# Optimization experiments

Measured on AMD Instinct MI355X. Metric: run time of the kernel, lower is better.

The kernel has to match this reference:

```python
import jax, jax.numpy as jnp
import numpy as np

B, T, N, C = 2, 3, 6, 16            # batch, time steps, cameras, frustum channels
FD, FH, FW = 48, 24, 64             # frustum depth bins, feature height, width
GX, GY, GZ = 100, 100, 8            # voxel grid size (X, Y, Z)
PC_MIN = np.array([-50.0, -50.0, -3.0], np.float32)
PC_MAX = np.array([50.0, 50.0, 5.0], np.float32)
D_MIN, D_MAX = 2.0, 46.8            # uniform depth discretization (UD)
OUT_CH = 40


def setup_inputs() -> dict:
    key = jax.random.key(0)
    ks = jax.random.split(key, 8)
    frustum_features = jax.random.normal(ks[0], (B, T, N, C, FD, FH, FW), jnp.float32)
    # camera looks along world +x so voxel points land in front of the camera
    base_rt = jnp.array([[0., -1., 0., 0.],
                         [0., 0., -1., 0.],
                         [1., 0., 0., 0.],
                         [0., 0., 0., 1.]], jnp.float32)
    RT = base_rt + 0.02 * jax.random.normal(ks[1], (B, T, N, 4, 4), jnp.float32)
    K = jnp.array([[32., 0., FW / 2.], [0., 32., FH / 2.], [0., 0., 1.]], jnp.float32)
    intrins = K + 0.1 * jax.random.normal(ks[2], (B, 3, 3), jnp.float32)
    DoF = jnp.eye(4, dtype=jnp.float32) + 0.01 * jax.random.normal(ks[3], (B, T, 4, 4), jnp.float32)
    W_N = 0.05 * jax.random.normal(ks[4], (OUT_CH, N * C), jnp.float32)
    b_N = jnp.zeros((OUT_CH,), jnp.float32)
    W_T = 0.05 * jax.random.normal(ks[5], (OUT_CH, T * OUT_CH), jnp.float32)
    b_T = jnp.zeros((OUT_CH,), jnp.float32)
    return {"frustum_features": frustum_features, "RT": RT, "intrins": intrins,
            "DoF": DoF, "W_N": W_N, "b_N": b_N, "W_T": W_T, "b_T": b_T}


def _grid_sample_3d(feat, grid):
    """Trilinear grid_sample. feat [M,C,D,H,W], grid [M,A,B2,C3,3] with
    normalized (x->W, y->H, z->D) coords, align_corners=True, zeros padding."""
    def one(f, g):
        _, Dd, Hh, Ww = f.shape
        ix = (g[..., 0] + 1.) * 0.5 * (Ww - 1)
        iy = (g[..., 1] + 1.) * 0.5 * (Hh - 1)
        iz = (g[..., 2] + 1.) * 0.5 * (Dd - 1)
        x0 = jnp.floor(ix); y0 = jnp.floor(iy); z0 = jnp.floor(iz)
        wx1 = ix - x0; wy1 = iy - y0; wz1 = iz - z0
        wx0 = 1. - wx1; wy0 = 1. - wy1; wz0 = 1. - wz1

        def corner(zf, yf, xf, w):
            valid = ((xf >= 0) & (xf <= Ww - 1) & (yf >= 0) & (yf <= Hh - 1)
                     & (zf >= 0) & (zf <= Dd - 1))
            zi = jnp.clip(zf, 0, Dd - 1).astype(jnp.int32)
            yi = jnp.clip(yf, 0, Hh - 1).astype(jnp.int32)
            xi = jnp.clip(xf, 0, Ww - 1).astype(jnp.int32)
            v = f[:, zi, yi, xi]                       # [C, A, B2, C3]
            return v * (w * valid)[None]

        return (corner(z0, y0, x0, wz0 * wy0 * wx0)
                + corner(z0, y0, x0 + 1, wz0 * wy0 * wx1)
                + corner(z0, y0 + 1, x0, wz0 * wy1 * wx0)
                + corner(z0, y0 + 1, x0 + 1, wz0 * wy1 * wx1)
                + corner(z0 + 1, y0, x0, wz1 * wy0 * wx0)
                + corner(z0 + 1, y0, x0 + 1, wz1 * wy0 * wx1)
                + corner(z0 + 1, y0 + 1, x0, wz1 * wy1 * wx0)
                + corner(z0 + 1, y0 + 1, x0 + 1, wz1 * wy1 * wx1))
    return jax.vmap(one)(feat, grid)


def _frustum_grid(intrins, RT):
    """Project voxel centers into (u, v, depth-bin) frustum coords, normalized to [-1,1]."""
    vs = (PC_MAX - PC_MIN) / np.array([GX, GY, GZ], np.float32)
    xs = PC_MIN[0] + (np.arange(GX, dtype=np.float32) + 0.5) * vs[0]
    ys = PC_MIN[1] + (np.arange(GY, dtype=np.float32) + 0.5) * vs[1]
    zs = PC_MIN[2] + (np.arange(GZ, dtype=np.float32) + 0.5) * vs[2]
    xx, yy, zz = np.meshgrid(xs, ys, zs, indexing='ij')
    pts = jnp.asarray(np.stack([xx, yy, zz, np.ones_like(xx)], -1))  # [GX,GY,GZ,4]
    cam = jnp.einsum('btnij,xyzj->btnxyzi', RT, pts)[..., :3]
    proj = jnp.einsum('bij,btnxyzj->btnxyzi', intrins, cam)
    zc = jnp.maximum(proj[..., 2], 1e-5)
    u = proj[..., 0] / zc
    v = proj[..., 1] / zc
    dbin = (proj[..., 2] - D_MIN) / ((D_MAX - D_MIN) / FD)
    gx = 2. * u / (FW - 1) - 1.
    gy = 2. * v / (FH - 1) - 1.
    gz = 2. * dbin / (FD - 1) - 1.
    return jnp.stack([gx, gy, gz], -1)  # [B,T,N,GX,GY,GZ,3]


def _affine_grid(theta, Dp, Hp, Wp):
    zs = np.linspace(-1., 1., Dp, dtype=np.float32)
    ys = np.linspace(-1., 1., Hp, dtype=np.float32)
    xs = np.linspace(-1., 1., Wp, dtype=np.float32)
    zz, yy, xx = np.meshgrid(zs, ys, xs, indexing='ij')
    base = jnp.asarray(np.stack([xx, yy, zz, np.ones_like(xx)], -1))  # [Dp,Hp,Wp,4]
    return jnp.einsum('bij,dhwj->bdhwi', theta, base)


def reference(frustum_features, RT, intrins, DoF, W_N, b_N, W_T, b_T):
    # --- per-time, per-camera frustum -> voxel sampling (batched over B*T*N) ---
    grids = _frustum_grid(intrins, RT)                                  # [B,T,N,GX,GY,GZ,3]
    feats = frustum_features.reshape(B * T * N, C, FD, FH, FW)
    gflat = grids.reshape(B * T * N, GX, GY, GZ, 3)
    vox = _grid_sample_3d(feats, gflat).reshape(B, T, N, C, GX, GY, GZ)
    vox = vox.transpose(0, 1, 2, 3, 4, 6, 5)                            # [B,T,N,C,GX,GZ,GY] (Y/Z swap from original permute)
    vox = vox.reshape(B, T, N * C, GX, GZ, GY)
    # --- Conv3DCollapse_N: 1x1x1 conv over cameras x channels + ReLU ---
    h = jax.nn.relu(jnp.einsum('oc,btcxyz->btoxyz', W_N, vox)
                    + b_N[None, None, :, None, None, None])             # [B,T,40,GX,GZ,GY]
    # --- cumulative temporal warp (trilinear grid_sample with affine pose grids) ---
    theta = DoF[:, :, 0:3, :]                                           # [B,T,3,4]
    bottom = jnp.broadcast_to(jnp.array([0., 0., 0., 1.], jnp.float32), (B, T, 1, 4))
    M4 = jnp.concatenate([theta, bottom], axis=2)                       # [B,T,4,4]
    Dp, Hp, Wp = GX, GZ, GY
    cum = jnp.broadcast_to(jnp.eye(4, dtype=jnp.float32), (B, 4, 4))
    outs = [None] * T
    for t in range(T - 1, -1, -1):                                      # small fixed T=3
        if t < T - 1:
            cum = jnp.einsum('bij,bjk->bik', M4[:, t], cum)
        g = _affine_grid(cum[:, :3, :], Dp, Hp, Wp)
        outs[t] = _grid_sample_3d(h[:, t], g)
    warped = jnp.stack(outs, axis=1)                                    # [B,T,40,Dp,Hp,Wp]
    flat = warped.reshape(B, T * OUT_CH, Dp, Hp, Wp)
    # --- Conv3DCollapse_T: 1x1x1 conv over time x channels + ReLU ---
    return jax.nn.relu(jnp.einsum('oc,bcxyz->boxyz', W_T, flat)
                       + b_T[None, :, None, None, None])
```

## Files before the change

kernel.cpp:

```cpp
#include <hip/hip_runtime.h>

#define NB 2
#define NT 3
#define NCAM 6
#define NC 16
#define FD 48
#define FH 24
#define FW 64
#define GX 100
#define GY 100
#define GZ 8
#define OC 40
#define NVOX (GX * GY * GZ)
#define FSZ (FD * FH * FW)
#define CAMSZ (NC * FSZ)
#define BTSZ (NCAM * CAMSZ)
#define HSZ ((size_t)NB * NT * OC * NVOX)
#define FT_ELEMS ((size_t)NB * NT * NCAM * FSZ * NC)

static __device__ __forceinline__ unsigned short f2bf_rne(float x) {
    unsigned int u = __float_as_uint(x);
    unsigned int r = (u + 0x7fffu + ((u >> 16) & 1u)) >> 16;
    return (unsigned short)r;
}
static __device__ __forceinline__ float bf_lo(unsigned int u) {
    return __uint_as_float(u << 16);
}
static __device__ __forceinline__ float bf_hi(unsigned int u) {
    return __uint_as_float(u & 0xffff0000u);
}

static __device__ __forceinline__ void do_setup(
    int tid, const float* __restrict__ RT, const float* __restrict__ intrins,
    const float* __restrict__ DoF, float* __restrict__ P,
    float* __restrict__ theta) {
    if (tid < NB * NT * NCAM) {
        int bt = tid / NCAM;
        int b = bt / NT;
        const float* I3 = intrins + b * 9;
        const float* R = RT + (size_t)tid * 16;
        float* Pp = P + tid * 12;
        for (int r = 0; r < 3; ++r)
            for (int c = 0; c < 4; ++c) {
                float s = 0.f;
                for (int k = 0; k < 3; ++k) s += I3[r * 3 + k] * R[k * 4 + c];
                Pp[r * 4 + c] = s;
            }
    }
    if (tid >= 64 && tid < 64 + NB) {
        int b = tid - 64;
        const float* D0 = DoF + (size_t)(b * NT + 0) * 16;
        const float* D1 = DoF + (size_t)(b * NT + 1) * 16;
        float* th = theta + (size_t)b * NT * 12;
        for (int i = 0; i < 12; ++i) th[2 * 12 + i] = 0.f;
        th[2 * 12 + 0] = 1.f; th[2 * 12 + 5] = 1.f; th[2 * 12 + 10] = 1.f;
        for (int i = 0; i < 12; ++i) th[1 * 12 + i] = D1[i];
        for (int r = 0; r < 3; ++r)
            for (int c = 0; c < 4; ++c) {
                float s = (c == 3) ? D0[r * 4 + 3] : 0.f;
                for (int k = 0; k < 3; ++k) s += D0[r * 4 + k] * D1[k * 4 + c];
                th[0 * 12 + r * 4 + c] = s;
            }
    }
}

__global__ void setup_kernel(const float* __restrict__ RT,
                             const float* __restrict__ intrins,
                             const float* __restrict__ DoF,
                             float* __restrict__ P,
                             float* __restrict__ theta) {
    do_setup(threadIdx.x, RT, intrins, DoF, P, theta);
}

template <typename FT>
__global__ __launch_bounds__(256) void transpose_feat(
    const float* __restrict__ feat, FT* __restrict__ ft,
    const float* __restrict__ RT, const float* __restrict__ intrins,
    const float* __restrict__ DoF, float* __restrict__ P,
    float* __restrict__ theta) {
    if (blockIdx.x == 0) do_setup(threadIdx.x, RT, intrins, DoF, P, theta);
    size_t tid = (size_t)blockIdx.x * 256 + threadIdx.x;
    int pos = (int)(tid % FSZ);
    int btn = (int)(tid / FSZ);
    const float* src = feat + (size_t)btn * CAMSZ + pos;
    float v[NC];
#pragma unroll
    for (int c = 0; c < NC; ++c) v[c] = src[(size_t)c * FSZ];
    if constexpr (sizeof(FT) == 4) {
        float4* dst = reinterpret_cast<float4*>(
            (float*)ft + ((size_t)btn * FSZ + pos) * NC);
#pragma unroll
        for (int q = 0; q < 4; ++q)
            dst[q] = make_float4(v[4 * q], v[4 * q + 1], v[4 * q + 2], v[4 * q + 3]);
    } else {
        unsigned int packed[8];
#pragma unroll
        for (int j = 0; j < 8; ++j)
            packed[j] = (unsigned int)f2bf_rne(v[2 * j]) |
                        ((unsigned int)f2bf_rne(v[2 * j + 1]) << 16);
        uint4* dst = reinterpret_cast<uint4*>(
            (unsigned short*)ft + ((size_t)btn * FSZ + pos) * NC);
        dst[0] = make_uint4(packed[0], packed[1], packed[2], packed[3]);
        dst[1] = make_uint4(packed[4], packed[5], packed[6], packed[7]);
    }
}

template <typename FT, bool CHLAST>
__global__ __launch_bounds__(256) void sample_mlp1(
    const float* __restrict__ feat,
    const FT* __restrict__ ft,
    const float* __restrict__ P,
    const float* __restrict__ W_N,
    const float* __restrict__ b_N,
    unsigned short* __restrict__ h) {
    int tid = blockIdx.x * 256 + threadIdx.x;
    int vid = tid % NVOX;
    int bt = __builtin_amdgcn_readfirstlane(tid / NVOX);
    int gy = vid % GY;
    int r2 = vid / GY;
    int gz = r2 % GZ;
    int gx = r2 / GZ;
    float X = (float)gx - 49.5f;
    float Y = (float)gy - 49.5f;
    float Z = (float)gz - 2.5f;

    float acc[OC];
#pragma unroll
    for (int o = 0; o < OC; ++o) acc[o] = b_N[o];

    for (int n = 0; n < NCAM; ++n) {
        const float* Pp = P + (bt * NCAM + n) * 12;
        float px = Pp[0] * X + Pp[1] * Y + Pp[2] * Z + Pp[3];
        float py = Pp[4] * X + Pp[5] * Y + Pp[6] * Z + Pp[7];
        float pz = Pp[8] * X + Pp[9] * Y + Pp[10] * Z + Pp[11];
        float zc = fmaxf(pz, 1e-5f);
        float ix = px / zc;
        float iy = py / zc;
        float iz = (pz - 2.0f) * (48.0f / 44.8f);

        bool cam_valid = (ix > -1.f) & (ix < (float)FW) &
                         (iy > -1.f) & (iy < (float)FH) &
                         (iz > -1.f) & (iz < (float)FD);
        if (!cam_valid) continue;

        float x0 = floorf(ix), y0 = floorf(iy), z0 = floorf(iz);
        float wx1 = ix - x0, wy1 = iy - y0, wz1 = iz - z0;
        float wx0 = 1.f - wx1, wy0 = 1.f - wy1, wz0 = 1.f - wz1;

        float w8[8];
        int off8[8];
#pragma unroll
        for (int k = 0; k < 8; ++k) {
            float xf = x0 + (float)(k & 1);
            float yf = y0 + (float)((k >> 1) & 1);
            float zf = z0 + (float)(k >> 2);
            bool valid = (xf >= 0.f) & (xf <= (float)(FW - 1)) &
                         (yf >= 0.f) & (yf <= (float)(FH - 1)) &
                         (zf >= 0.f) & (zf <= (float)(FD - 1));
            int xi = (int)fminf(fmaxf(xf, 0.f), (float)(FW - 1));
            int yi = (int)fminf(fmaxf(yf, 0.f), (float)(FH - 1));
            int zi = (int)fminf(fmaxf(zf, 0.f), (float)(FD - 1));
            float w = ((k & 1) ? wx1 : wx0) * (((k >> 1) & 1) ? wy1 : wy0) *
                      ((k >> 2) ? wz1 : wz0);
            w8[k] = valid ? w : 0.f;
            off8[k] = (zi * FH + yi) * FW + xi;
        }

        float s[NC];
#pragma unroll
        for (int c = 0; c < NC; ++c) s[c] = 0.f;

        if constexpr (CHLAST) {
            const size_t camBase = (size_t)(bt * NCAM + n) * FSZ;
            if constexpr (sizeof(FT) == 4) {
#pragma unroll
                for (int k = 0; k < 8; ++k) {
                    float w = w8[k];
                    const float4* cp = reinterpret_cast<const float4*>(
                        (const float*)ft + (camBase + (size_t)off8[k]) * NC);
#pragma unroll
                    for (int q = 0; q < 4; ++q) {
                        float4 v = cp[q];
                        s[4 * q + 0] = fmaf(w, v.x, s[4 * q + 0]);
                        s[4 * q + 1] = fmaf(w, v.y, s[4 * q + 1]);
                        s[4 * q + 2] = fmaf(w, v.z, s[4 * q + 2]);
                        s[4 * q + 3] = fmaf(w, v.w, s[4 * q + 3]);
                    }
                }
            } else {
#pragma unroll
                for (int k = 0; k < 8; ++k) {
                    float w = w8[k];
                    const uint4* cp = reinterpret_cast<const uint4*>(
                        (const unsigned short*)ft + (camBase + (size_t)off8[k]) * NC);
                    uint4 a = cp[0], b2 = cp[1];
                    unsigned int uu[8] = {a.x, a.y, a.z, a.w, b2.x, b2.y, b2.z, b2.w};
#pragma unroll
                    for (int j = 0; j < 8; ++j) {
                        s[2 * j + 0] = fmaf(w, bf_lo(uu[j]), s[2 * j + 0]);
                        s[2 * j + 1] = fmaf(w, bf_hi(uu[j]), s[2 * j + 1]);
                    }
                }
            }
        } else {
            const float* fn = feat + (size_t)bt * BTSZ + (size_t)n * CAMSZ;
#pragma unroll
            for (int c = 0; c < NC; ++c) {
                const float* fc = fn + (size_t)c * FSZ;
                float v = 0.f;
#pragma unroll
                for (int k = 0; k < 8; ++k) v = fmaf(w8[k], fc[off8[k]], v);
                s[c] = v;
            }
        }

#pragma unroll
        for (int o = 0; o < OC; ++o) {
            const float4* w4 =
                reinterpret_cast<const float4*>(W_N + o * (NCAM * NC) + n * NC);
#pragma unroll
            for (int q = 0; q < 4; ++q) {
                float4 w = w4[q];
                acc[o] = fmaf(w.x, s[4 * q + 0], acc[o]);
                acc[o] = fmaf(w.y, s[4 * q + 1], acc[o]);
                acc[o] = fmaf(w.z, s[4 * q + 2], acc[o]);
                acc[o] = fmaf(w.w, s[4 * q + 3], acc[o]);
            }
        }
    }

    unsigned int u[20];
#pragma unroll
    for (int j = 0; j < 20; ++j)
        u[j] = (unsigned int)f2bf_rne(fmaxf(acc[2 * j], 0.f)) |
               ((unsigned int)f2bf_rne(fmaxf(acc[2 * j + 1], 0.f)) << 16);
    uint4* d4 = reinterpret_cast<uint4*>(
        h + ((size_t)bt * NVOX + (size_t)vid) * OC);
#pragma unroll
    for (int q = 0; q < 5; ++q)
        d4[q] = make_uint4(u[4 * q], u[4 * q + 1], u[4 * q + 2], u[4 * q + 3]);
}

__global__ __launch_bounds__(256) void warp_mlp2(
    const unsigned short* __restrict__ h,
    const float* __restrict__ theta,
    const float* __restrict__ W_T,
    const float* __restrict__ b_T,
    float* __restrict__ out) {
    int tid = blockIdx.x * 256 + threadIdx.x;
    int vid = tid % NVOX;
    int b = __builtin_amdgcn_readfirstlane(tid / NVOX);
    int w_ = vid % GY;
    int r2 = vid / GY;
    int h_ = r2 % GZ;
    int d_ = r2 / GZ;

    float xg = -1.f + 2.f * (float)w_ / 99.f;
    float yg = -1.f + 2.f * (float)h_ / 7.f;
    float zg = -1.f + 2.f * (float)d_ / 99.f;

    float acc[OC];
#pragma unroll
    for (int o = 0; o < OC; ++o) acc[o] = b_T[o];

    for (int t = 0; t < 2; ++t) {
        const float* th = theta + (b * NT + t) * 12;
        float g0 = th[0] * xg + th[1] * yg + th[2] * zg + th[3];
        float g1 = th[4] * xg + th[5] * yg + th[6] * zg + th[7];
        float g2 = th[8] * xg + th[9] * yg + th[10] * zg + th[11];
        float ix = (g0 + 1.f) * 0.5f * 99.f;
        float iy = (g1 + 1.f) * 0.5f * 7.f;
        float iz = (g2 + 1.f) * 0.5f * 99.f;
        float x0 = floorf(ix), y0 = floorf(iy), z0 = floorf(iz);
        float wx1 = ix - x0, wy1 = iy - y0, wz1 = iz - z0;
        float wx0 = 1.f - wx1, wy0 = 1.f - wy1, wz0 = 1.f - wz1;

        float w8[8];
        int off8[8];
#pragma unroll
        for (int k = 0; k < 8; ++k) {
            float xf = x0 + (float)(k & 1);
            float yf = y0 + (float)((k >> 1) & 1);
            float zf = z0 + (float)(k >> 2);
            bool valid = (xf >= 0.f) & (xf <= 99.f) &
                         (yf >= 0.f) & (yf <= 7.f) &
                         (zf >= 0.f) & (zf <= 99.f);
            int xi = (int)fminf(fmaxf(xf, 0.f), 99.f);
            int yi = (int)fminf(fmaxf(yf, 0.f), 7.f);
            int zi = (int)fminf(fmaxf(zf, 0.f), 99.f);
            float w = ((k & 1) ? wx1 : wx0) * (((k >> 1) & 1) ? wy1 : wy0) *
                      ((k >> 2) ? wz1 : wz0);
            w8[k] = valid ? w : 0.f;
            off8[k] = (zi * GZ + yi) * GY + xi;
        }

        const unsigned short* hb = h + (size_t)(b * NT + t) * NVOX * OC;
        float sval[OC];
#pragma unroll
        for (int o2 = 0; o2 < OC; ++o2) sval[o2] = 0.f;
#pragma unroll
        for (int k = 0; k < 8; ++k) {
            float w = w8[k];
            const uint4* cp =
                reinterpret_cast<const uint4*>(hb + (size_t)off8[k] * OC);
            uint4 a0 = cp[0], a1 = cp[1], a2 = cp[2], a3 = cp[3], a4 = cp[4];
            unsigned int uu[20] = {a0.x, a0.y, a0.z, a0.w, a1.x, a1.y, a1.z, a1.w,
                                   a2.x, a2.y, a2.z, a2.w, a3.x, a3.y, a3.z, a3.w,
                                   a4.x, a4.y, a4.z, a4.w};
#pragma unroll
            for (int j = 0; j < 20; ++j) {
                sval[2 * j + 0] = fmaf(w, bf_lo(uu[j]), sval[2 * j + 0]);
                sval[2 * j + 1] = fmaf(w, bf_hi(uu[j]), sval[2 * j + 1]);
            }
        }

#pragma unroll
        for (int o = 0; o < OC; ++o) {
            const float4* w4 =
                reinterpret_cast<const float4*>(W_T + o * (NT * OC) + t * OC);
#pragma unroll
            for (int q = 0; q < 10; ++q) {
                float4 w = w4[q];
                acc[o] = fmaf(w.x, sval[4 * q + 0], acc[o]);
                acc[o] = fmaf(w.y, sval[4 * q + 1], acc[o]);
                acc[o] = fmaf(w.z, sval[4 * q + 2], acc[o]);
                acc[o] = fmaf(w.w, sval[4 * q + 3], acc[o]);
            }
        }
    }

    {
        const uint4* cp = reinterpret_cast<const uint4*>(
            h + ((size_t)(b * NT + 2) * NVOX + (size_t)vid) * OC);
        uint4 a0 = cp[0], a1 = cp[1], a2 = cp[2], a3 = cp[3], a4 = cp[4];
        unsigned int uu[20] = {a0.x, a0.y, a0.z, a0.w, a1.x, a1.y, a1.z, a1.w,
                               a2.x, a2.y, a2.z, a2.w, a3.x, a3.y, a3.z, a3.w,
                               a4.x, a4.y, a4.z, a4.w};
        float sval[OC];
#pragma unroll
        for (int j = 0; j < 20; ++j) {
            sval[2 * j + 0] = bf_lo(uu[j]);
            sval[2 * j + 1] = bf_hi(uu[j]);
        }
#pragma unroll
        for (int o = 0; o < OC; ++o) {
            const float4* w4 =
                reinterpret_cast<const float4*>(W_T + o * (NT * OC) + 2 * OC);
#pragma unroll
            for (int q = 0; q < 10; ++q) {
                float4 w = w4[q];
                acc[o] = fmaf(w.x, sval[4 * q + 0], acc[o]);
                acc[o] = fmaf(w.y, sval[4 * q + 1], acc[o]);
                acc[o] = fmaf(w.z, sval[4 * q + 2], acc[o]);
                acc[o] = fmaf(w.w, sval[4 * q + 3], acc[o]);
            }
        }
    }

    float* op = out + (size_t)b * OC * NVOX + vid;
#pragma unroll
    for (int o = 0; o < OC; ++o) op[(size_t)o * NVOX] = fmaxf(acc[o], 0.f);
}

extern "C" void kernel_launch(void* const* d_in, const int* in_sizes, int n_in,
                              void* d_out, int out_size, void* d_ws, size_t ws_size,
                              hipStream_t stream) {
    const float* frustum = (const float*)d_in[0];
    const float* RT      = (const float*)d_in[1];
    const float* intrins = (const float*)d_in[2];
    const float* DoF     = (const float*)d_in[3];
    const float* W_N     = (const float*)d_in[4];
    const float* b_N     = (const float*)d_in[5];
    const float* W_T     = (const float*)d_in[6];
    const float* b_T     = (const float*)d_in[7];
    float* out = (float*)d_out;

    const size_t ft_f32  = FT_ELEMS * sizeof(float);
    const size_t ft_bf16 = FT_ELEMS * sizeof(unsigned short);
    const size_t h_bytes = HSZ * sizeof(unsigned short);
    const size_t small = 4096;

    char* base = (char*)d_ws;
    int mode;
    size_t ft_bytes;
    if (ws_size >= ft_f32 + h_bytes + small) { mode = 0; ft_bytes = ft_f32; }
    else if (ws_size >= ft_bf16 + h_bytes + small) { mode = 1; ft_bytes = ft_bf16; }
    else { mode = 2; ft_bytes = 0; }

    size_t ft_al = (ft_bytes + 255) & ~(size_t)255;
    void* ft_buf = base;
    unsigned short* h_buf = (unsigned short*)(base + ft_al);
    float* P_buf = (float*)(base + ft_al + ((h_bytes + 255) & ~(size_t)255));
    float* th_buf = P_buf + NB * NT * NCAM * 12;

    const int tr_blocks = (NB * NT * NCAM * FSZ) / 256;
    const int n1_blocks = (NB * NT * NVOX) / 256;
    const int n2_blocks = (NB * NVOX) / 256;

    if (mode == 0) {
        transpose_feat<float><<<tr_blocks, 256, 0, stream>>>(
            frustum, (float*)ft_buf, RT, intrins, DoF, P_buf, th_buf);
        sample_mlp1<float, true><<<n1_blocks, 256, 0, stream>>>(
            frustum, (const float*)ft_buf, P_buf, W_N, b_N, h_buf);
    } else if (mode == 1) {
        transpose_feat<unsigned short><<<tr_blocks, 256, 0, stream>>>(
            frustum, (unsigned short*)ft_buf, RT, intrins, DoF, P_buf, th_buf);
        sample_mlp1<unsigned short, true><<<n1_blocks, 256, 0, stream>>>(
            frustum, (const unsigned short*)ft_buf, P_buf, W_N, b_N, h_buf);
    } else {
        setup_kernel<<<1, 128, 0, stream>>>(RT, intrins, DoF, P_buf, th_buf);
        sample_mlp1<float, false><<<n1_blocks, 256, 0, stream>>>(
            frustum, (const float*)nullptr, P_buf, W_N, b_N, h_buf);
    }

    warp_mlp2<<<n2_blocks, 256, 0, stream>>>(h_buf, th_buf, W_T, b_T, out);
}
```

Baseline: 459.7 us.

## Batch gather loads ahead of use, add XCD block swizzle and occupancy hint

In warp_mlp2, the loads for all eight trilinear corners are issued up front into a register array before the accumulation loop, and the t=2 passthrough row is prefetched at kernel start. The goal is more memory-level parallelism so gather latency is hidden. Both kernels also remap block IDs so that consecutive blocks land on the same XCD, which should improve L2 locality. A launch-bounds minimum of 2 blocks is added to warp_mlp2, and together with the 160+ extra live registers this risks spilling or register-pressure limits.

```diff
diff --git a/kernel.cpp b/kernel.cpp
--- a/kernel.cpp
+++ b/kernel.cpp
@@ -30,6 +30,13 @@
     return __uint_as_float(u & 0xffff0000u);
 }
 
+static __device__ __forceinline__ int xcd_swizzle(int bid, int nwg) {
+    int xcd = bid & 7;
+    int local = bid >> 3;
+    int q = nwg >> 3, r = nwg & 7;
+    return (xcd < r ? xcd * (q + 1) : r * (q + 1) + (xcd - r) * q) + local;
+}
+
 static __device__ __forceinline__ void do_setup(
     int tid, const float* __restrict__ RT, const float* __restrict__ intrins,
     const float* __restrict__ DoF, float* __restrict__ P,
@@ -113,7 +120,8 @@
     const float* __restrict__ W_N,
     const float* __restrict__ b_N,
     unsigned short* __restrict__ h) {
-    int tid = blockIdx.x * 256 + threadIdx.x;
+    int bid = xcd_swizzle(blockIdx.x, gridDim.x);
+    int tid = bid * 256 + threadIdx.x;
     int vid = tid % NVOX;
     int bt = __builtin_amdgcn_readfirstlane(tid / NVOX);
     int gy = vid % GY;
@@ -241,13 +249,14 @@
         d4[q] = make_uint4(u[4 * q], u[4 * q + 1], u[4 * q + 2], u[4 * q + 3]);
 }
 
-__global__ __launch_bounds__(256) void warp_mlp2(
+__global__ __launch_bounds__(256, 2) void warp_mlp2(
     const unsigned short* __restrict__ h,
     const float* __restrict__ theta,
     const float* __restrict__ W_T,
     const float* __restrict__ b_T,
     float* __restrict__ out) {
-    int tid = blockIdx.x * 256 + threadIdx.x;
+    int bid = xcd_swizzle(blockIdx.x, gridDim.x);
+    int tid = bid * 256 + threadIdx.x;
     int vid = tid % NVOX;
     int b = __builtin_amdgcn_readfirstlane(tid / NVOX);
     int w_ = vid % GY;
@@ -258,6 +267,14 @@
     float xg = -1.f + 2.f * (float)w_ / 99.f;
     float yg = -1.f + 2.f * (float)h_ / 7.f;
     float zg = -1.f + 2.f * (float)d_ / 99.f;
+
+    uint4 p2[5];
+    {
+        const uint4* cp2 = reinterpret_cast<const uint4*>(
+            h + ((size_t)(b * NT + 2) * NVOX + (size_t)vid) * OC);
+#pragma unroll
+        for (int q = 0; q < 5; ++q) p2[q] = cp2[q];
+    }
 
     float acc[OC];
 #pragma unroll
@@ -295,22 +312,33 @@
         }
 
         const unsigned short* hb = h + (size_t)(b * NT + t) * NVOX * OC;
+
+        uint4 rr[8][5];
+#pragma unroll
+        for (int k = 0; k < 8; ++k) {
+            const uint4* cp =
+                reinterpret_cast<const uint4*>(hb + (size_t)off8[k] * OC);
+#pragma unroll
+            for (int q = 0; q < 5; ++q) rr[k][q] = cp[q];
+        }
+
         float sval[OC];
 #pragma unroll
         for (int o2 = 0; o2 < OC; ++o2) sval[o2] = 0.f;
 #pragma unroll
         for (int k = 0; k < 8; ++k) {
             float w = w8[k];
-            const uint4* cp =
-                reinterpret_cast<const uint4*>(hb + (size_t)off8[k] * OC);
-            uint4 a0 = cp[0], a1 = cp[1], a2 = cp[2], a3 = cp[3], a4 = cp[4];
-            unsigned int uu[20] = {a0.x, a0.y, a0.z, a0.w, a1.x, a1.y, a1.z, a1.w,
-                                   a2.x, a2.y, a2.z, a2.w, a3.x, a3.y, a3.z, a3.w,
-                                   a4.x, a4.y, a4.z, a4.w};
-#pragma unroll
-            for (int j = 0; j < 20; ++j) {
-                sval[2 * j + 0] = fmaf(w, bf_lo(uu[j]), sval[2 * j + 0]);
-                sval[2 * j + 1] = fmaf(w, bf_hi(uu[j]), sval[2 * j + 1]);
+#pragma unroll
+            for (int q = 0; q < 5; ++q) {
+                uint4 a = rr[k][q];
+                sval[8 * q + 0] = fmaf(w, bf_lo(a.x), sval[8 * q + 0]);
+                sval[8 * q + 1] = fmaf(w, bf_hi(a.x), sval[8 * q + 1]);
+                sval[8 * q + 2] = fmaf(w, bf_lo(a.y), sval[8 * q + 2]);
+                sval[8 * q + 3] = fmaf(w, bf_hi(a.y), sval[8 * q + 3]);
+                sval[8 * q + 4] = fmaf(w, bf_lo(a.z), sval[8 * q + 4]);
+                sval[8 * q + 5] = fmaf(w, bf_hi(a.z), sval[8 * q + 5]);
+                sval[8 * q + 6] = fmaf(w, bf_lo(a.w), sval[8 * q + 6]);
+                sval[8 * q + 7] = fmaf(w, bf_hi(a.w), sval[8 * q + 7]);
             }
         }
 
@@ -330,17 +358,18 @@
     }
 
     {
-        const uint4* cp = reinterpret_cast<const uint4*>(
-            h + ((size_t)(b * NT + 2) * NVOX + (size_t)vid) * OC);
-        uint4 a0 = cp[0], a1 = cp[1], a2 = cp[2], a3 = cp[3], a4 = cp[4];
-        unsigned int uu[20] = {a0.x, a0.y, a0.z, a0.w, a1.x, a1.y, a1.z, a1.w,
-                               a2.x, a2.y, a2.z, a2.w, a3.x, a3.y, a3.z, a3.w,
-                               a4.x, a4.y, a4.z, a4.w};
         float sval[OC];
 #pragma unroll
-        for (int j = 0; j < 20; ++j) {
-            sval[2 * j + 0] = bf_lo(uu[j]);
-            sval[2 * j + 1] = bf_hi(uu[j]);
+        for (int q = 0; q < 5; ++q) {
+            uint4 a = p2[q];
+            sval[8 * q + 0] = bf_lo(a.x);
+            sval[8 * q + 1] = bf_hi(a.x);
+            sval[8 * q + 2] = bf_lo(a.y);
+            sval[8 * q + 3] = bf_hi(a.y);
+            sval[8 * q + 4] = bf_lo(a.z);
+            sval[8 * q + 5] = bf_hi(a.z);
+            sval[8 * q + 6] = bf_lo(a.w);
+            sval[8 * q + 7] = bf_hi(a.w);
         }
 #pragma unroll
         for (int o = 0; o < OC; ++o) {
```

Measured after the change: 580.6 us. 1.26x slower.
